# Kernel optimization log

Hardware: AMD Instinct MI355X
Metric: run time of the kernel (lower is better)

Reference implementation:

```python
import jax, jax.numpy as jnp
import numpy as np

RES = 16; NC = 256; NCP = 1024; KNN = 32; SIGMA = 0.1
DM = 256; NH = 8; FF = 1024; NLAYERS = 2
E = NC * 8 * (RES // 8) ** 2
EH = 8
B = 4; N = 65536


def setup_inputs() -> dict:
    key = jax.random.key(0)
    ks = jax.random.split(key, 16)
    s = 0.02
    def w(k, shape):
        return jax.random.normal(k, shape, jnp.float32) * s
    inp = {}
    inp['pc'] = jax.random.normal(ks[0], (B, N, 3), jnp.float32)
    inp['pe_w1'] = w(ks[1], (3, 128)); inp['pe_b1'] = jnp.zeros((128,), jnp.float32)
    inp['pe_w2'] = w(ks[2], (128, 128)); inp['pe_b2'] = jnp.zeros((128,), jnp.float32)
    inp['t_qkv_w'] = w(ks[3], (NLAYERS, DM, 3 * DM)); inp['t_qkv_b'] = jnp.zeros((NLAYERS, 3 * DM), jnp.float32)
    inp['t_out_w'] = w(ks[4], (NLAYERS, DM, DM)); inp['t_out_b'] = jnp.zeros((NLAYERS, DM), jnp.float32)
    inp['t_ln1_s'] = jnp.ones((NLAYERS, DM), jnp.float32); inp['t_ln1_b'] = jnp.zeros((NLAYERS, DM), jnp.float32)
    inp['t_ff1_w'] = w(ks[5], (NLAYERS, DM, FF)); inp['t_ff1_b'] = jnp.zeros((NLAYERS, FF), jnp.float32)
    inp['t_ff2_w'] = w(ks[6], (NLAYERS, FF, DM)); inp['t_ff2_b'] = jnp.zeros((NLAYERS, DM), jnp.float32)
    inp['t_ln2_s'] = jnp.ones((NLAYERS, DM), jnp.float32); inp['t_ln2_b'] = jnp.zeros((NLAYERS, DM), jnp.float32)
    inp['c1_w'] = w(ks[7], (2 * NC, NC, 3, 3)); inp['c1_b'] = jnp.zeros((2 * NC,), jnp.float32)
    inp['c2_w'] = w(ks[8], (4 * NC, 2 * NC, 3, 3)); inp['c2_b'] = jnp.zeros((4 * NC,), jnp.float32)
    inp['c3_w'] = w(ks[9], (8 * NC, 4 * NC, 3, 3)); inp['c3_b'] = jnp.zeros((8 * NC,), jnp.float32)
    inp['x_qkv_w'] = w(ks[10], (E, 3 * E)); inp['x_qkv_b'] = jnp.zeros((3 * E,), jnp.float32)
    inp['x_out_w'] = w(ks[11], (E, E)); inp['x_out_b'] = jnp.zeros((E,), jnp.float32)
    return inp


def _layernorm(x, s, b):
    m = x.mean(-1, keepdims=True)
    v = ((x - m) ** 2).mean(-1, keepdims=True)
    return (x - m) / jnp.sqrt(v + 1e-5) * s + b


def _mha(x, qkv_w, qkv_b, out_w, out_b, nh):
    Bq, S, D = x.shape
    dh = D // nh
    qkv = x @ qkv_w + qkv_b
    q, k, v = jnp.split(qkv, 3, axis=-1)
    def sp(t):
        return t.reshape(Bq, S, nh, dh).transpose(0, 2, 1, 3)
    q, k, v = sp(q), sp(k), sp(v)
    a = jax.nn.softmax(jnp.einsum('bhqd,bhkd->bhqk', q, k) / jnp.sqrt(jnp.float32(dh)), axis=-1)
    o = jnp.einsum('bhqk,bhkd->bhqd', a, v).transpose(0, 2, 1, 3).reshape(Bq, S, D)
    return o @ out_w + out_b


def _density(pc):
    # faithful to source: distance to the FIRST k points (unsorted), not kNN
    d = jnp.linalg.norm(pc[:, :, None, :] - pc[:, None, :KNN, :], axis=-1)  # (B,N,k)
    return jnp.exp(-2.0 * SIGMA ** 2 / (d * d + 1e-6)).mean(axis=-1)


def _fps_indices(pc, density):
    # incremental min-dist FPS: selects identical points to the original O(N*K^2) loop
    def one(pc_b, dens_b):
        first = jnp.argmax(dens_b)
        mind = jnp.linalg.norm(pc_b - pc_b[first], axis=-1)
        def step(mind, _):
            idx = jnp.argmax(mind)
            d = jnp.linalg.norm(pc_b - pc_b[idx], axis=-1)
            return jnp.minimum(mind, d), idx
        _, rest = jax.lax.scan(step, mind, None, length=NCP - 1)
        return jnp.concatenate([first[None], rest])
    return jax.vmap(one)(pc, density)


def _forward(pc, idx, pe_w1, pe_b1, pe_w2, pe_b2, t_qkv_w, t_qkv_b, t_out_w, t_out_b,
             t_ln1_s, t_ln1_b, t_ff1_w, t_ff1_b, t_ff2_w, t_ff2_b, t_ln2_s, t_ln2_b,
             c1_w, c1_b, c2_w, c2_b, c3_w, c3_b, x_qkv_w, x_qkv_b, x_out_w, x_out_b):
    Bq = pc.shape[0]
    centers = jnp.take_along_axis(pc, idx[:, :, None], axis=1)  # (B,K,3)
    # point encoder MLP -> (B,K,128)
    f = jax.nn.relu(centers @ pe_w1 + pe_b1) @ pe_w2 + pe_b2
    # sinusoidal pos-emb per axis, mean over xyz -> (B,K,128)
    half = 64
    freqs = jnp.exp(jnp.arange(half, dtype=jnp.float32) * (-np.log(10000.0) / (half - 1)))
    e = centers[..., None] * freqs  # (B,K,3,64)
    pos = jnp.concatenate([jnp.sin(e), jnp.cos(e)], axis=-1).mean(axis=2)
    x = jnp.concatenate([f, pos], axis=-1)  # (B,K,256)
    # 2-layer post-LN transformer encoder
    for l in range(NLAYERS):
        h = _mha(x, t_qkv_w[l], t_qkv_b[l], t_out_w[l], t_out_b[l], NH)
        x = _layernorm(x + h, t_ln1_s[l], t_ln1_b[l])
        h = jax.nn.relu(x @ t_ff1_w[l] + t_ff1_b[l]) @ t_ff2_w[l] + t_ff2_b[l]
        x = _layernorm(x + h, t_ln2_s[l], t_ln2_b[l])
    # scatter-add features onto three planes
    L = pc.max() - pc.min()
    def grid(c):
        return jnp.clip(((c + L / 2) / L * RES).astype(jnp.int32), 0, RES - 1)
    gx = grid(centers[..., 0]); gy = grid(centers[..., 1]); gz = grid(centers[..., 2])
    tri = jnp.zeros((Bq, 3, RES, RES, DM), jnp.float32)  # channels last for scatter
    bi = jnp.arange(Bq)[:, None]
    tri = tri.at[bi, 0, gy, gx].add(x)
    tri = tri.at[bi, 1, gz, gy].add(x)
    tri = tri.at[bi, 2, gz, gx].add(x)
    tri = tri.transpose(0, 1, 4, 2, 3)  # (B,3,C,R,R)
    z = tri.reshape(Bq * 3, DM, RES, RES)
    def conv(xx, w, b):
        y = jax.lax.conv_general_dilated(xx, w, (2, 2), ((1, 1), (1, 1)),
                                         dimension_numbers=('NCHW', 'OIHW', 'NCHW'))
        return y + b[None, :, None, None]
    z = jax.nn.relu(conv(z, c1_w, c1_b))
    z = jax.nn.relu(conv(z, c2_w, c2_b))
    z = jax.nn.relu(conv(z, c3_w, c3_b))  # (B*3, 8C, R/8, R/8)
    flat = z.reshape(Bq, 3, E)
    attn = _mha(flat, x_qkv_w, x_qkv_b, x_out_w, x_out_b, EH)
    return attn.reshape(Bq, 3, 8 * NC, RES // 8, RES // 8)


def reference(pc, pe_w1, pe_b1, pe_w2, pe_b2, t_qkv_w, t_qkv_b, t_out_w, t_out_b,
              t_ln1_s, t_ln1_b, t_ff1_w, t_ff1_b, t_ff2_w, t_ff2_b, t_ln2_s, t_ln2_b,
              c1_w, c1_b, c2_w, c2_b, c3_w, c3_b, x_qkv_w, x_qkv_b, x_out_w, x_out_b):
    idx = _fps_indices(pc, _density(pc))
    return _forward(pc, idx, pe_w1, pe_b1, pe_w2, pe_b2, t_qkv_w, t_qkv_b, t_out_w, t_out_b,
                    t_ln1_s, t_ln1_b, t_ff1_w, t_ff1_b, t_ff2_w, t_ff2_b, t_ln2_s, t_ln2_b,
                    c1_w, c1_b, c2_w, c2_b, c3_w, c3_b, x_qkv_w, x_qkv_b, x_out_w, x_out_b)
```

## Files before the change

kernel.cpp:

```cpp
#include <hip/hip_runtime.h>
#include <math.h>

#define NPTS   65536
#define NBATCH 4
#define KCP    1024
#define DM     256
#define FFD    1024
#define EDIM   8192
#define N3E    24576

#define FPS_NBLK 16
#define FPS_THR  256
#define FPS_PPT  16
#define GPUB     8
#define HARV_MAX 16
#define RING     16
#define TSPLIT   512

typedef __attribute__((ext_vector_type(8))) short short8v;
typedef __attribute__((ext_vector_type(4))) short short4v;
typedef __attribute__((ext_vector_type(4))) float float4v;

__device__ __forceinline__ unsigned long long umaxll(unsigned long long a, unsigned long long b) {
  return a > b ? a : b;
}

__device__ __forceinline__ short bf16rn(float f) {
  unsigned u = __float_as_uint(f);
  return (short)((u + 0x7FFFu + ((u >> 16) & 1u)) >> 16);
}

__global__ __launch_bounds__(256) void redmm_kernel(const float* __restrict__ v, int n,
                                                    float* __restrict__ pmax, float* __restrict__ pmin) {
  float mx = -INFINITY, mn = INFINITY;
  for (int i = blockIdx.x * 256 + threadIdx.x; i < n; i += gridDim.x * 256) {
    float x = v[i]; mx = fmaxf(mx, x); mn = fminf(mn, x);
  }
#pragma unroll
  for (int off = 32; off >= 1; off >>= 1) {
    mx = fmaxf(mx, __shfl_xor(mx, off, 64));
    mn = fminf(mn, __shfl_xor(mn, off, 64));
  }
  __shared__ float smx[4], smn[4];
  int lane = threadIdx.x & 63, w = threadIdx.x >> 6;
  if (lane == 0) { smx[w] = mx; smn[w] = mn; }
  __syncthreads();
  if (threadIdx.x == 0) {
    pmax[blockIdx.x] = fmaxf(fmaxf(smx[0], smx[1]), fmaxf(smx[2], smx[3]));
    pmin[blockIdx.x] = fminf(fminf(smn[0], smn[1]), fminf(smn[2], smn[3]));
  }
}

__global__ __launch_bounds__(256) void redfin_kernel(const float* __restrict__ pmax,
                                                     const float* __restrict__ pmin, int nb,
                                                     float* __restrict__ Lv) {
  float mx = -INFINITY, mn = INFINITY;
  for (int i = threadIdx.x; i < nb; i += 256) { mx = fmaxf(mx, pmax[i]); mn = fminf(mn, pmin[i]); }
#pragma unroll
  for (int off = 32; off >= 1; off >>= 1) {
    mx = fmaxf(mx, __shfl_xor(mx, off, 64));
    mn = fminf(mn, __shfl_xor(mn, off, 64));
  }
  __shared__ float smx[4], smn[4];
  int lane = threadIdx.x & 63, w = threadIdx.x >> 6;
  if (lane == 0) { smx[w] = mx; smn[w] = mn; }
  __syncthreads();
  if (threadIdx.x == 0) {
    mx = fmaxf(fmaxf(smx[0], smx[1]), fmaxf(smx[2], smx[3]));
    mn = fminf(fminf(smn[0], smn[1]), fminf(smn[2], smn[3]));
    Lv[0] = __fsub_rn(mx, mn);
  }
}

__global__ __launch_bounds__(FPS_THR, 1) void fps_kernel(const float* __restrict__ pc,
                                                         float* __restrict__ centers,
                                                         unsigned* __restrict__ tags,
                                                         unsigned long long* __restrict__ keys,
                                                         float* __restrict__ mindbuf,
                                                         int* __restrict__ state,
                                                         int phase) {
  const int blk = blockIdx.x;
  const int b = blk / FPS_NBLK, bb = blk % FPS_NBLK;
  const int tid = threadIdx.x;
  const int lane = tid & 63, wv = tid >> 6;
  const int wvg = bb * 4 + wv;
  const float* pcb = pc + (size_t)b * NPTS * 3;

  __shared__ float kpts[96];
  __shared__ float wlds[2][HARV_MAX][3];
  __shared__ int hcnt[2];

  float px[FPS_PPT], py[FPS_PPT], pz[FPS_PPT], mind[FPS_PPT];
  const int gbase = wvg * 1024;
#pragma unroll
  for (int i = 0; i < FPS_PPT; ++i) {
    int g = gbase + i * 64 + lane;
    px[i] = pcb[3 * g]; py[i] = pcb[3 * g + 1]; pz[i] = pcb[3 * g + 2];
  }

  unsigned* const tagb = tags + (size_t)b * RING * 64;
  unsigned long long* const keyb = keys + (size_t)b * RING * 64 * GPUB;
  float* const mb = mindbuf + ((size_t)b * 64 + wvg) * FPS_PPT * 64;

  int t, r;
  if (phase == 0) {
    for (int i = tid; i < 96; i += FPS_THR) kpts[i] = pcb[i];
    __syncthreads();
    unsigned long long bk = 0ull;
#pragma unroll
    for (int i = 0; i < FPS_PPT; ++i) {
      float acc = 0.f;
      for (int j = 0; j < 32; ++j) {
        float dx = __fsub_rn(px[i], kpts[3 * j]);
        float dy = __fsub_rn(py[i], kpts[3 * j + 1]);
        float dz = __fsub_rn(pz[i], kpts[3 * j + 2]);
        float ss = __fadd_rn(__fadd_rn(__fmul_rn(dx, dx), __fmul_rn(dy, dy)), __fmul_rn(dz, dz));
        float d = __fsqrt_rn(ss);
        float dd = __fadd_rn(__fmul_rn(d, d), 1e-6f);
        acc = __fadd_rn(acc, expf(__fdiv_rn(-0.02f, dd)));
      }
      float dens = __fdiv_rn(acc, 32.f);
      int g = gbase + i * 64 + lane;
      bk = umaxll(bk, ((unsigned long long)__float_as_uint(dens) << 32) | (unsigned int)(~g));
    }
#pragma unroll
    for (int off = 1; off < 64; off <<= 1) bk = umaxll(bk, __shfl_xor(bk, off, 64));
    if (lane == 0) {
      keyb[(size_t)(1 & (RING - 1)) * 64 * GPUB + wvg * GPUB] = bk;
      __hip_atomic_store(&tagb[(1 & (RING - 1)) * 64 + wvg], 1u, __ATOMIC_RELEASE, __HIP_MEMORY_SCOPE_AGENT);
    }
    unsigned tag;
    do {
      tag = __hip_atomic_load(&tagb[(1 & (RING - 1)) * 64 + lane], __ATOMIC_ACQUIRE, __HIP_MEMORY_SCOPE_AGENT);
    } while (__any(tag != 1u));
    unsigned long long k2 = __hip_atomic_load(&keyb[(size_t)(1 & (RING - 1)) * 64 * GPUB + lane * GPUB],
                                              __ATOMIC_RELAXED, __HIP_MEMORY_SCOPE_AGENT);
#pragma unroll
    for (int off = 1; off < 64; off <<= 1) k2 = umaxll(k2, __shfl_xor(k2, off, 64));
    int widx = (int)(~(unsigned)(k2 & 0xFFFFFFFFull));
    float wx = pcb[3 * widx], wy = pcb[3 * widx + 1], wz = pcb[3 * widx + 2];
    if (wvg == 0 && lane == 0) {
      centers[(size_t)b * KCP * 3 + 0] = wx;
      centers[(size_t)b * KCP * 3 + 1] = wy;
      centers[(size_t)b * KCP * 3 + 2] = wz;
    }
#pragma unroll
    for (int i = 0; i < FPS_PPT; ++i) {
      float dx = __fsub_rn(px[i], wx), dy = __fsub_rn(py[i], wy), dz = __fsub_rn(pz[i], wz);
      mind[i] = __fsqrt_rn(__fadd_rn(__fadd_rn(__fmul_rn(dx, dx), __fmul_rn(dy, dy)), __fmul_rn(dz, dz)));
    }
    t = 1; r = 2;
  } else {
    r = state[b * 2]; t = state[b * 2 + 1];
#pragma unroll
    for (int i = 0; i < FPS_PPT; ++i) mind[i] = mb[i * 64 + lane];
  }

  const int tend = phase ? KCP : TSPLIT;
  while (t < tend) {
    unsigned long long tk[FPS_PPT];
#pragma unroll
    for (int i = 0; i < FPS_PPT; ++i) {
      int g = gbase + i * 64 + lane;
      tk[i] = ((unsigned long long)__float_as_uint(mind[i]) << 32) | (unsigned int)(~g);
    }
    unsigned long long ek[GPUB];
#pragma unroll
    for (int g = 0; g < GPUB; ++g) {
      unsigned long long lbk = 0ull;
#pragma unroll
      for (int i = 0; i < FPS_PPT; ++i) lbk = umaxll(lbk, tk[i]);
      unsigned long long wk = lbk;
#pragma unroll
      for (int off = 1; off < 64; off <<= 1) wk = umaxll(wk, __shfl_xor(wk, off, 64));
      ek[g] = wk;
#pragma unroll
      for (int i = 0; i < FPS_PPT; ++i)
        if (tk[i] == wk) tk[i] = 0ull;
    }
    const int ri = r & (RING - 1);
    if (lane == 0) {
      unsigned long long* sp = keyb + ((size_t)ri * 64 + wvg) * GPUB;
#pragma unroll
      for (int g = 0; g < GPUB; ++g)
        __hip_atomic_store(&sp[g], ek[g], __ATOMIC_RELAXED, __HIP_MEMORY_SCOPE_AGENT);
      __hip_atomic_store(&tagb[ri * 64 + wvg], (unsigned)r, __ATOMIC_RELEASE, __HIP_MEMORY_SCOPE_AGENT);
    }

    if (wv == 0) {
      unsigned tag;
      do {
        tag = __hip_atomic_load(&tagb[ri * 64 + lane], __ATOMIC_ACQUIRE, __HIP_MEMORY_SCOPE_AGENT);
      } while (__any(tag != (unsigned)r));
      const unsigned long long* pl = keyb + ((size_t)ri * 64 + lane) * GPUB;
      unsigned long long ck[GPUB];
#pragma unroll
      for (int e = 0; e < GPUB; ++e)
        ck[e] = __hip_atomic_load(&pl[e], __ATOMIC_RELAXED, __HIP_MEMORY_SCOPE_AGENT);
      float cx[GPUB], cy[GPUB], cz[GPUB];
#pragma unroll
      for (int e = 0; e < GPUB; ++e) {
        int gi = (int)(~(unsigned)(ck[e] & 0xFFFFFFFFull));
        cx[e] = pcb[3 * gi]; cy[e] = pcb[3 * gi + 1]; cz[e] = pcb[3 * gi + 2];
      }
      unsigned long long u = ck[GPUB - 1];
#pragma unroll
      for (int off = 1; off < 64; off <<= 1) u = umaxll(u, __shfl_xor(u, off, 64));
      int h = 0, tl = t;
      while (true) {
        unsigned long long lb = 0ull; float lx = 0.f, ly = 0.f, lz = 0.f;
#pragma unroll
        for (int e = 0; e < GPUB; ++e)
          if (ck[e] > lb) { lb = ck[e]; lx = cx[e]; ly = cy[e]; lz = cz[e]; }
        unsigned long long wk = lb;
#pragma unroll
        for (int off = 1; off < 64; off <<= 1) wk = umaxll(wk, __shfl_xor(wk, off, 64));
        if (h > 0 && wk < u) break;
        int owner = __ffsll(__ballot(lb == wk)) - 1;
        float wx = __shfl(lx, owner, 64), wy = __shfl(ly, owner, 64), wz = __shfl(lz, owner, 64);
        if (lane == 0) {
          wlds[r & 1][h][0] = wx; wlds[r & 1][h][1] = wy; wlds[r & 1][h][2] = wz;
          if (bb == 0) {
            centers[((size_t)b * KCP + tl) * 3 + 0] = wx;
            centers[((size_t)b * KCP + tl) * 3 + 1] = wy;
            centers[((size_t)b * KCP + tl) * 3 + 2] = wz;
          }
        }
#pragma unroll
        for (int e = 0; e < GPUB; ++e) {
          float dx = __fsub_rn(cx[e], wx), dy = __fsub_rn(cy[e], wy), dz = __fsub_rn(cz[e], wz);
          float d = __fsqrt_rn(__fadd_rn(__fadd_rn(__fmul_rn(dx, dx), __fmul_rn(dy, dy)), __fmul_rn(dz, dz)));
          float ov = __uint_as_float((unsigned)(ck[e] >> 32));
          float nv = fminf(ov, d);
          ck[e] = ((unsigned long long)__float_as_uint(nv) << 32) | (ck[e] & 0xFFFFFFFFull);
        }
        ++h; ++tl;
        if (h == HARV_MAX || tl == KCP) break;
      }
      if (lane == 0) hcnt[r & 1] = h;
    }
    __syncthreads();
    const int h = hcnt[r & 1];
    for (int j = 0; j < h; ++j) {
      float wx = wlds[r & 1][j][0], wy = wlds[r & 1][j][1], wz = wlds[r & 1][j][2];
#pragma unroll
      for (int i = 0; i < FPS_PPT; ++i) {
        float dx = __fsub_rn(px[i], wx), dy = __fsub_rn(py[i], wy), dz = __fsub_rn(pz[i], wz);
        float d = __fsqrt_rn(__fadd_rn(__fadd_rn(__fmul_rn(dx, dx), __fmul_rn(dy, dy)), __fmul_rn(dz, dz)));
        mind[i] = fminf(mind[i], d);
      }
    }
    t += h; ++r;
  }

  if (phase == 0) {
#pragma unroll
    for (int i = 0; i < FPS_PPT; ++i) mb[i * 64 + lane] = mind[i];
    if (bb == 0 && wv == 0 && lane == 0) { state[b * 2] = r; state[b * 2 + 1] = t; }
  }
}

__global__ __launch_bounds__(128) void pe_kernel(const float* __restrict__ centers,
                                                 const float* __restrict__ w1, const float* __restrict__ b1,
                                                 const float* __restrict__ w2, const float* __restrict__ b2,
                                                 float* __restrict__ x) {
  const int p = blockIdx.x;
  const int d = threadIdx.x;
  __shared__ float h[128];
  __shared__ float c[3];
  if (d < 3) c[d] = centers[(size_t)p * 3 + d];
  __syncthreads();
  float hv = b1[d];
#pragma unroll
  for (int j = 0; j < 3; ++j) hv += c[j] * w1[j * 128 + d];
  hv = fmaxf(hv, 0.f);
  h[d] = hv;
  __syncthreads();
  float f = b2[d];
  for (int j = 0; j < 128; ++j) f += h[j] * w2[j * 128 + d];
  x[(size_t)p * 256 + d] = f;
  if (d < 64) {
    float fr = expf(__fmul_rn((float)d, -0.14619587892025696f));
    float ssum = 0.f, csum = 0.f;
#pragma unroll
    for (int a = 0; a < 3; ++a) {
      float e = __fmul_rn(c[a], fr);
      ssum += sinf(e); csum += cosf(e);
    }
    x[(size_t)p * 256 + 128 + d] = __fdiv_rn(ssum, 3.f);
    x[(size_t)p * 256 + 192 + d] = __fdiv_rn(csum, 3.f);
  }
}

__global__ __launch_bounds__(256) void gemm_mfma_kernel(const float* __restrict__ A,
                                                        const float* __restrict__ W,
                                                        const float* __restrict__ bias,
                                                        float* __restrict__ C,
                                                        int M, int Kd, int Nd, int relu) {
  __shared__ __align__(16) short Al[128][40];
  __shared__ __align__(16) short Wl[128][40];
  const int bm = blockIdx.y * 128, bn = blockIdx.x * 128;
  const int tid = threadIdx.x;
  const int lane = tid & 63, wv = tid >> 6;
  const int wr = wv >> 1, wc = wv & 1;
  const int l15 = lane & 15, lk = lane >> 4;

  float4v acc[4][4];
#pragma unroll
  for (int i = 0; i < 4; ++i)
#pragma unroll
    for (int j = 0; j < 4; ++j) acc[i][j] = (float4v){0.f, 0.f, 0.f, 0.f};

  for (int k0 = 0; k0 < Kd; k0 += 32) {
    __syncthreads();
#pragma unroll
    for (int i = 0; i < 4; ++i) {
      int idx = (i * 256 + tid) * 4;
      int m = idx >> 5, k = idx & 31;
      float4 v = *(const float4*)&A[(size_t)(bm + m) * Kd + k0 + k];
      short4v s = { bf16rn(v.x), bf16rn(v.y), bf16rn(v.z), bf16rn(v.w) };
      *(short4v*)&Al[m][k] = s;
    }
#pragma unroll
    for (int i = 0; i < 4; ++i) {
      int task = i * 256 + tid;
      int n = task & 127, c = task >> 7;
      short4v s;
#pragma unroll
      for (int j = 0; j < 4; ++j)
        s[j] = bf16rn(W[(size_t)(k0 + c * 4 + j) * Nd + bn + n]);
      *(short4v*)&Wl[n][c * 4] = s;
    }
    __syncthreads();
    short8v af[4], bf[4];
#pragma unroll
    for (int mf = 0; mf < 4; ++mf)
      af[mf] = *(const short8v*)&Al[wr * 64 + mf * 16 + l15][lk * 8];
#pragma unroll
    for (int nf = 0; nf < 4; ++nf)
      bf[nf] = *(const short8v*)&Wl[wc * 64 + nf * 16 + l15][lk * 8];
#pragma unroll
    for (int mf = 0; mf < 4; ++mf)
#pragma unroll
      for (int nf = 0; nf < 4; ++nf)
        acc[mf][nf] = __builtin_amdgcn_mfma_f32_16x16x32_bf16(af[mf], bf[nf], acc[mf][nf], 0, 0, 0);
  }

#pragma unroll
  for (int mf = 0; mf < 4; ++mf) {
    int row = bm + wr * 64 + mf * 16 + lk * 4;
#pragma unroll
    for (int nf = 0; nf < 4; ++nf) {
      int col = bn + wc * 64 + nf * 16 + l15;
      float bv = bias[col];
#pragma unroll
      for (int j = 0; j < 4; ++j) {
        float v = acc[mf][nf][j] + bv;
        if (relu) v = fmaxf(v, 0.f);
        C[(size_t)(row + j) * Nd + col] = v;
      }
    }
  }
}

__global__ __launch_bounds__(256, 1) void flash_mfma_kernel(const float* __restrict__ qkv,
                                                            float* __restrict__ ao) {
  const int qt = blockIdx.x, h = blockIdx.y, b = blockIdx.z;
  const int tid = threadIdx.x;
  const int lane = tid & 63, w = tid >> 6;
  const int l15 = lane & 15, lk = lane >> 4;
  const int q0 = qt * 64;

  __shared__ __align__(16) short Kc[64][40];
  __shared__ __align__(16) short Vt[32][72];
  __shared__ __align__(16) short Plds[4][16][72];

  short8v qa;
  {
    const float* qr = qkv + (size_t)(b * 1024 + q0 + w * 16 + l15) * 768 + h * 32 + lk * 8;
    float4 a = *(const float4*)qr;
    float4 c = *(const float4*)(qr + 4);
    qa = (short8v){ bf16rn(a.x), bf16rn(a.y), bf16rn(a.z), bf16rn(a.w),
                    bf16rn(c.x), bf16rn(c.y), bf16rn(c.z), bf16rn(c.w) };
  }

  float4v o0 = (float4v){0.f, 0.f, 0.f, 0.f};
  float4v o1 = (float4v){0.f, 0.f, 0.f, 0.f};
  float m_cur[4] = { -INFINITY, -INFINITY, -INFINITY, -INFINITY };
  float l_part[4] = { 0.f, 0.f, 0.f, 0.f };
  const float scale = 0.17677669529663687f;

  for (int c0 = 0; c0 < 1024; c0 += 64) {
    __syncthreads();
    {
      int key = tid >> 2, dblk = (tid & 3) * 8;
      size_t row = (size_t)(b * 1024 + c0 + key) * 768 + h * 32 + dblk;
      float4 k1 = *(const float4*)&qkv[row + 256];
      float4 k2 = *(const float4*)&qkv[row + 260];
      short8v ks = (short8v){ bf16rn(k1.x), bf16rn(k1.y), bf16rn(k1.z), bf16rn(k1.w),
                              bf16rn(k2.x), bf16rn(k2.y), bf16rn(k2.z), bf16rn(k2.w) };
      *(short8v*)&Kc[key][dblk] = ks;
      float4 v1 = *(const float4*)&qkv[row + 512];
      float4 v2 = *(const float4*)&qkv[row + 516];
      Vt[dblk + 0][key] = bf16rn(v1.x); Vt[dblk + 1][key] = bf16rn(v1.y);
      Vt[dblk + 2][key] = bf16rn(v1.z); Vt[dblk + 3][key] = bf16rn(v1.w);
      Vt[dblk + 4][key] = bf16rn(v2.x); Vt[dblk + 5][key] = bf16rn(v2.y);
      Vt[dblk + 6][key] = bf16rn(v2.z); Vt[dblk + 7][key] = bf16rn(v2.w);
    }
    __syncthreads();

    float4v s[4];
#pragma unroll
    for (int f = 0; f < 4; ++f) {
      short8v kb = *(const short8v*)&Kc[f * 16 + l15][lk * 8];
      float4v z = (float4v){0.f, 0.f, 0.f, 0.f};
      s[f] = __builtin_amdgcn_mfma_f32_16x16x32_bf16(qa, kb, z, 0, 0, 0);
    }
#pragma unroll
    for (int f = 0; f < 4; ++f)
#pragma unroll
      for (int j = 0; j < 4; ++j) s[f][j] *= scale;

    float corr[4];
#pragma unroll
    for (int j = 0; j < 4; ++j) {
      float v = fmaxf(fmaxf(s[0][j], s[1][j]), fmaxf(s[2][j], s[3][j]));
#pragma unroll
      for (int off = 1; off < 16; off <<= 1) v = fmaxf(v, __shfl_xor(v, off, 64));
      float m_new = fmaxf(m_cur[j], v);
      corr[j] = expf(m_cur[j] - m_new);
      m_cur[j] = m_new;
    }
#pragma unroll
    for (int f = 0; f < 4; ++f)
#pragma unroll
      for (int j = 0; j < 4; ++j) {
        float p = expf(s[f][j] - m_cur[j]);
        s[f][j] = p;
        Plds[w][lk * 4 + j][f * 16 + l15] = bf16rn(p);
      }
#pragma unroll
    for (int j = 0; j < 4; ++j) {
      float tsum = s[0][j] + s[1][j] + s[2][j] + s[3][j];
#pragma unroll
      for (int off = 1; off < 16; off <<= 1) tsum += __shfl_xor(tsum, off, 64);
      l_part[j] = l_part[j] * corr[j] + tsum;
      o0[j] *= corr[j];
      o1[j] *= corr[j];
    }
    asm volatile("s_waitcnt lgkmcnt(0)" ::: "memory");
    __builtin_amdgcn_sched_barrier(0);

#pragma unroll
    for (int kb = 0; kb < 2; ++kb) {
      short8v pa = *(const short8v*)&Plds[w][l15][kb * 32 + lk * 8];
      short8v vb0 = *(const short8v*)&Vt[l15][kb * 32 + lk * 8];
      short8v vb1 = *(const short8v*)&Vt[16 + l15][kb * 32 + lk * 8];
      o0 = __builtin_amdgcn_mfma_f32_16x16x32_bf16(pa, vb0, o0, 0, 0, 0);
      o1 = __builtin_amdgcn_mfma_f32_16x16x32_bf16(pa, vb1, o1, 0, 0, 0);
    }
  }

#pragma unroll
  for (int j = 0; j < 4; ++j) {
    float inv = 1.f / l_part[j];
    int q = q0 + w * 16 + lk * 4 + j;
    float* orow = ao + (size_t)(b * 1024 + q) * 256 + h * 32;
    orow[l15] = o0[j] * inv;
    orow[16 + l15] = o1[j] * inv;
  }
}

__global__ __launch_bounds__(256) void ln_kernel(const float* __restrict__ a, const float* __restrict__ r,
                                                 const float* __restrict__ sc, const float* __restrict__ bi,
                                                 float* __restrict__ out) {
  const int row = blockIdx.x * 4 + (threadIdx.x >> 6);
  const int lane = threadIdx.x & 63;
  const float* ar = a + (size_t)row * 256;
  const float* rr = r + (size_t)row * 256;
  float v[4];
#pragma unroll
  for (int i = 0; i < 4; ++i) v[i] = ar[lane + 64 * i] + rr[lane + 64 * i];
  float s = v[0] + v[1] + v[2] + v[3];
#pragma unroll
  for (int off = 32; off >= 1; off >>= 1) s += __shfl_xor(s, off, 64);
  float mean = s * (1.f / 256.f);
  float vs = 0.f;
#pragma unroll
  for (int i = 0; i < 4; ++i) { float d = v[i] - mean; vs += d * d; }
#pragma unroll
  for (int off = 32; off >= 1; off >>= 1) vs += __shfl_xor(vs, off, 64);
  float var = vs * (1.f / 256.f);
  float rstd = 1.f / sqrtf(var + 1e-5f);
  float* orow = out + (size_t)row * 256;
#pragma unroll
  for (int i = 0; i < 4; ++i) {
    int d = lane + 64 * i;
    orow[d] = (v[i] - mean) * rstd * sc[d] + bi[d];
  }
}

__global__ __launch_bounds__(256) void scatter_kernel(const float* __restrict__ x,
                                                      const float* __restrict__ centers,
                                                      const float* __restrict__ Lv,
                                                      float* __restrict__ tri) {
  const int pnt = blockIdx.x;
  const int b = pnt >> 10;
  const int tid = threadIdx.x;
  __shared__ int g[3];
  if (tid == 0) {
    float L = Lv[0];
    float half = __fmul_rn(L, 0.5f);
#pragma unroll
    for (int a = 0; a < 3; ++a) {
      float c = centers[(size_t)pnt * 3 + a];
      float t = __fmul_rn(__fdiv_rn(__fadd_rn(c, half), L), 16.f);
      int gi = (int)t;
      g[a] = min(15, max(0, gi));
    }
  }
  __syncthreads();
  const int gx = g[0], gy = g[1], gz = g[2];
  float v = x[(size_t)pnt * 256 + tid];
  float* trib = tri + (size_t)b * 3 * 256 * 256;
  atomicAdd(&trib[(0 * 256 + tid) * 256 + gy * 16 + gx], v);
  atomicAdd(&trib[(1 * 256 + tid) * 256 + gz * 16 + gy], v);
  atomicAdd(&trib[(2 * 256 + tid) * 256 + gz * 16 + gx], v);
}

template <int IC, int OC, int IH, int IW, int OH, int OW, int OCT, int ICC>
__global__ __launch_bounds__(256, 1) void conv_kernel(const float* __restrict__ in, const float* __restrict__ w,
                                                      const float* __restrict__ bias, float* __restrict__ out) {
  __shared__ float lin[ICC * IH * IW];
  const int n = blockIdx.x;
  const int oc = blockIdx.y * OCT + threadIdx.x / (OH * OW);
  const int sp = threadIdx.x % (OH * OW);
  const int oy = sp / OW, ox = sp % OW;
  const int iy0 = oy * 2 - 1, ix0 = ox * 2 - 1;
  float acc = 0.f;
  for (int c0 = 0; c0 < IC; c0 += ICC) {
    __syncthreads();
    for (int i = threadIdx.x; i < ICC * IH * IW; i += 256)
      lin[i] = in[((size_t)n * IC + c0) * (IH * IW) + i];
    __syncthreads();
    const float* wp = w + ((size_t)oc * IC + c0) * 9;
    for (int ic = 0; ic < ICC; ++ic) {
      const float* wr = wp + (size_t)ic * 9;
      const float* lr = lin + ic * IH * IW;
#pragma unroll
      for (int ky = 0; ky < 3; ++ky) {
        int iy = iy0 + ky;
        if (iy >= 0 && iy < IH) {
#pragma unroll
          for (int kx = 0; kx < 3; ++kx) {
            int ix = ix0 + kx;
            if (ix >= 0 && ix < IW) acc += lr[iy * IW + ix] * wr[ky * 3 + kx];
          }
        }
      }
    }
  }
  out[((size_t)n * OC + oc) * (OH * OW) + sp] = fmaxf(acc + bias[oc], 0.f);
}

template <int M, int KC>
__global__ __launch_bounds__(256, 1) void matvec_part_kernel(const float* __restrict__ A,
                                                             const float* __restrict__ W,
                                                             float* __restrict__ part,
                                                             int Kd, int Nd) {
  __shared__ float Al[KC * M];
  const int tid = threadIdx.x;
  const int n = blockIdx.x * 256 + tid;
  const int k0 = blockIdx.y * KC;
  for (int i = tid; i < KC * M; i += 256) {
    int k = i / M, m = i - k * M;
    Al[i] = A[(size_t)m * Kd + k0 + k];
  }
  __syncthreads();
  float acc[M] = {};
  for (int k = 0; k < KC; ++k) {
    float wv = W[(size_t)(k0 + k) * Nd + n];
#pragma unroll
    for (int m = 0; m < M; ++m) acc[m] += Al[k * M + m] * wv;
  }
  float* pp = part + ((size_t)blockIdx.y * M) * Nd;
#pragma unroll
  for (int m = 0; m < M; ++m) pp[(size_t)m * Nd + n] = acc[m];
}

__global__ __launch_bounds__(256) void redsum_kernel(const float* __restrict__ part,
                                                     const float* __restrict__ bias,
                                                     float* __restrict__ out, int Nd, int total) {
  int i = blockIdx.x * 256 + threadIdx.x;
  if (i < total) {
    int n = i % Nd;
    float s = bias[n];
#pragma unroll
    for (int c = 0; c < 16; ++c) s += part[(size_t)c * total + i];
    out[i] = s;
  }
}

__global__ __launch_bounds__(256) void attn3_kernel(const float* __restrict__ qkv, float* __restrict__ o) {
  const int b = blockIdx.x >> 3, h = blockIdx.x & 7;
  const float* base = qkv + (size_t)b * 3 * N3E;
  const int qo = h * 1024, ko = EDIM + h * 1024, vo = 2 * EDIM + h * 1024;
  float p[9] = {};
  for (int d = threadIdx.x; d < 1024; d += 256) {
    float q0 = base[qo + d], q1 = base[N3E + qo + d], q2 = base[2 * N3E + qo + d];
    float k0 = base[ko + d], k1 = base[N3E + ko + d], k2 = base[2 * N3E + ko + d];
    p[0] += q0 * k0; p[1] += q0 * k1; p[2] += q0 * k2;
    p[3] += q1 * k0; p[4] += q1 * k1; p[5] += q1 * k2;
    p[6] += q2 * k0; p[7] += q2 * k1; p[8] += q2 * k2;
  }
  __shared__ float red[4][9];
  __shared__ float aw[9];
  const int lane = threadIdx.x & 63, w = threadIdx.x >> 6;
#pragma unroll
  for (int e = 0; e < 9; ++e)
#pragma unroll
    for (int off = 32; off >= 1; off >>= 1) p[e] += __shfl_xor(p[e], off, 64);
  if (lane == 0)
#pragma unroll
    for (int e = 0; e < 9; ++e) red[w][e] = p[e];
  __syncthreads();
  if (threadIdx.x == 0) {
    float s[9];
#pragma unroll
    for (int e = 0; e < 9; ++e) s[e] = (red[0][e] + red[1][e] + red[2][e] + red[3][e]) / 32.f;
#pragma unroll
    for (int i = 0; i < 3; ++i) {
      float m = fmaxf(fmaxf(s[i * 3], s[i * 3 + 1]), s[i * 3 + 2]);
      float e0 = expf(s[i * 3] - m), e1 = expf(s[i * 3 + 1] - m), e2 = expf(s[i * 3 + 2] - m);
      float sm = e0 + e1 + e2;
      aw[i * 3] = e0 / sm; aw[i * 3 + 1] = e1 / sm; aw[i * 3 + 2] = e2 / sm;
    }
  }
  __syncthreads();
  for (int d = threadIdx.x; d < 1024; d += 256) {
    float v0 = base[vo + d], v1 = base[N3E + vo + d], v2 = base[2 * N3E + vo + d];
#pragma unroll
    for (int i = 0; i < 3; ++i)
      o[(size_t)(b * 3 + i) * EDIM + h * 1024 + d] = aw[i * 3] * v0 + aw[i * 3 + 1] * v1 + aw[i * 3 + 2] * v2;
  }
}

extern "C" void kernel_launch(void* const* d_in, const int* in_sizes, int n_in,
                              void* d_out, int out_size, void* d_ws, size_t ws_size,
                              hipStream_t stream) {
  const float* pc      = (const float*)d_in[0];
  const float* pe_w1   = (const float*)d_in[1];
  const float* pe_b1   = (const float*)d_in[2];
  const float* pe_w2   = (const float*)d_in[3];
  const float* pe_b2   = (const float*)d_in[4];
  const float* t_qkv_w = (const float*)d_in[5];
  const float* t_qkv_b = (const float*)d_in[6];
  const float* t_out_w = (const float*)d_in[7];
  const float* t_out_b = (const float*)d_in[8];
  const float* t_ln1_s = (const float*)d_in[9];
  const float* t_ln1_b = (const float*)d_in[10];
  const float* t_ff1_w = (const float*)d_in[11];
  const float* t_ff1_b = (const float*)d_in[12];
  const float* t_ff2_w = (const float*)d_in[13];
  const float* t_ff2_b = (const float*)d_in[14];
  const float* t_ln2_s = (const float*)d_in[15];
  const float* t_ln2_b = (const float*)d_in[16];
  const float* c1_w    = (const float*)d_in[17];
  const float* c1_b    = (const float*)d_in[18];
  const float* c2_w    = (const float*)d_in[19];
  const float* c2_b    = (const float*)d_in[20];
  const float* c3_w    = (const float*)d_in[21];
  const float* c3_b    = (const float*)d_in[22];
  const float* x_qkv_w = (const float*)d_in[23];
  const float* x_qkv_b = (const float*)d_in[24];
  const float* x_out_w = (const float*)d_in[25];
  const float* x_out_b = (const float*)d_in[26];
  float* outp = (float*)d_out;

  char* wsp = (char*)d_ws;
  auto alloc = [&](size_t bytes) { char* q = wsp; wsp += (bytes + 255) & ~(size_t)255; return q; };
  float* centers = (float*)alloc((size_t)NBATCH * KCP * 3 * 4);
  float* pmax    = (float*)alloc(512 * 4);
  float* pmin    = (float*)alloc(512 * 4);
  float* Lv      = (float*)alloc(256);
  unsigned* tags = (unsigned*)alloc((size_t)NBATCH * RING * 64 * 4);
  unsigned long long* keyss = (unsigned long long*)alloc((size_t)NBATCH * RING * 64 * GPUB * 8);
  float* mindbuf = (float*)alloc((size_t)NBATCH * NPTS * 4);
  int* fstate    = (int*)alloc(256);
  float* x  = (float*)alloc((size_t)4096 * 256 * 4);
  float* xb = (float*)alloc((size_t)4096 * 256 * 4);
  float* arena = (float*)wsp;
  float* qkvb = arena;
  float* ao   = qkvb + (size_t)4096 * 768;
  float* po   = ao + (size_t)4096 * 256;
  float* ffh  = po + (size_t)4096 * 256;
  float* ffo  = ffh + (size_t)4096 * 1024;
  float* tri  = arena;
  float* z1   = tri + (size_t)NBATCH * 3 * 256 * 256;
  float* z2   = z1 + (size_t)12 * 512 * 64;
  float* z3   = z2 + (size_t)12 * 1024 * 16;
  float* qkv2 = z3 + (size_t)12 * 8192;
  float* at2  = qkv2 + (size_t)12 * N3E;
  float* mvp  = at2 + (size_t)12 * EDIM;
  (void)in_sizes; (void)n_in; (void)out_size; (void)ws_size; (void)ffo;

  hipMemsetAsync(tags, 0, (size_t)NBATCH * RING * 64 * 4 + (size_t)NBATCH * RING * 64 * GPUB * 8, stream);

  redmm_kernel<<<512, 256, 0, stream>>>(pc, NBATCH * NPTS * 3, pmax, pmin);
  redfin_kernel<<<1, 256, 0, stream>>>(pmax, pmin, 512, Lv);

  fps_kernel<<<NBATCH * FPS_NBLK, FPS_THR, 0, stream>>>(pc, centers, tags, keyss, mindbuf, fstate, 0);
  fps_kernel<<<NBATCH * FPS_NBLK, FPS_THR, 0, stream>>>(pc, centers, tags, keyss, mindbuf, fstate, 1);

  pe_kernel<<<NBATCH * KCP, 128, 0, stream>>>(centers, pe_w1, pe_b1, pe_w2, pe_b2, x);

  for (int l = 0; l < 2; ++l) {
    gemm_mfma_kernel<<<dim3(6, 32), 256, 0, stream>>>(x, t_qkv_w + (size_t)l * 256 * 768,
                                                      t_qkv_b + (size_t)l * 768, qkvb, 4096, 256, 768, 0);
    flash_mfma_kernel<<<dim3(16, 8, 4), 256, 0, stream>>>(qkvb, ao);
    gemm_mfma_kernel<<<dim3(2, 32), 256, 0, stream>>>(ao, t_out_w + (size_t)l * 256 * 256,
                                                      t_out_b + (size_t)l * 256, po, 4096, 256, 256, 0);
    ln_kernel<<<1024, 256, 0, stream>>>(x, po, t_ln1_s + (size_t)l * 256, t_ln1_b + (size_t)l * 256, xb);
    gemm_mfma_kernel<<<dim3(8, 32), 256, 0, stream>>>(xb, t_ff1_w + (size_t)l * 256 * 1024,
                                                      t_ff1_b + (size_t)l * 1024, ffh, 4096, 256, 1024, 1);
    gemm_mfma_kernel<<<dim3(2, 32), 256, 0, stream>>>(ffh, t_ff2_w + (size_t)l * 1024 * 256,
                                                      t_ff2_b + (size_t)l * 256, ffo, 4096, 1024, 256, 0);
    ln_kernel<<<1024, 256, 0, stream>>>(xb, ffo, t_ln2_s + (size_t)l * 256, t_ln2_b + (size_t)l * 256, x);
  }

  hipMemsetAsync(tri, 0, (size_t)NBATCH * 3 * 256 * 256 * 4, stream);
  scatter_kernel<<<NBATCH * KCP, 256, 0, stream>>>(x, centers, Lv, tri);

  conv_kernel<256, 512, 16, 16, 8, 8, 4, 32><<<dim3(12, 128), 256, 0, stream>>>(tri, c1_w, c1_b, z1);
  conv_kernel<512, 1024, 8, 8, 4, 4, 16, 128><<<dim3(12, 64), 256, 0, stream>>>(z1, c2_w, c2_b, z2);
  conv_kernel<1024, 2048, 4, 4, 2, 2, 64, 256><<<dim3(12, 32), 256, 0, stream>>>(z2, c3_w, c3_b, z3);

  matvec_part_kernel<12, 512><<<dim3(N3E / 256, 16), 256, 0, stream>>>(z3, x_qkv_w, mvp, EDIM, N3E);
  redsum_kernel<<<(12 * N3E + 255) / 256, 256, 0, stream>>>(mvp, x_qkv_b, qkv2, N3E, 12 * N3E);

  attn3_kernel<<<32, 256, 0, stream>>>(qkv2, at2);

  matvec_part_kernel<12, 512><<<dim3(EDIM / 256, 16), 256, 0, stream>>>(at2, x_out_w, mvp, EDIM, EDIM);
  redsum_kernel<<<(12 * EDIM + 255) / 256, 256, 0, stream>>>(mvp, x_out_b, outp, EDIM, 12 * EDIM);
}
```

Before: 4.503 ms.

## Restructure conv3 to reuse weights across batch and vectorize matvec weight loads

The third conv layer gets its own kernel. Each thread owns one output channel and spatial position and accumulates all 12 images, staging input channel slices in shared memory so each weight is loaded once and reused 12 times. The matvec kernels now read weights as float4 and each thread handles four output columns, which cuts grid size by four. This targets the weight-bandwidth-bound tail, but the conv3 grid shrinks to 32 blocks and the matvec to 24 or 8 by 16 blocks, so far fewer CUs may be occupied.

```diff
diff --git a/kernel.cpp b/kernel.cpp
--- a/kernel.cpp
+++ b/kernel.cpp
@@ -563,29 +563,84 @@
   out[((size_t)n * OC + oc) * (OH * OW) + sp] = fmaxf(acc + bias[oc], 0.f);
 }
 
+__global__ __launch_bounds__(256, 1) void conv3w_kernel(const float* __restrict__ in,
+                                                        const float* __restrict__ w,
+                                                        const float* __restrict__ bias,
+                                                        float* __restrict__ out) {
+  __shared__ float lin[12][128][16];
+  const int oc = blockIdx.x * 64 + (threadIdx.x >> 2);
+  const int sp = threadIdx.x & 3;
+  const int oy = sp >> 1, ox = sp & 1;
+  const int iy0 = oy * 2 - 1, ix0 = ox * 2 - 1;
+  float acc[12] = {};
+  for (int c0 = 0; c0 < 1024; c0 += 128) {
+    __syncthreads();
+    for (int i = threadIdx.x; i < 6144; i += 256) {
+      int n = i / 512, r4 = i - n * 512;
+      ((float4*)&lin[n][0][0])[r4] = ((const float4*)(in + ((size_t)n * 1024 + c0) * 16))[r4];
+    }
+    __syncthreads();
+    const float* wp = w + ((size_t)oc * 1024 + c0) * 9;
+    for (int ic = 0; ic < 128; ++ic) {
+      const float* wr = wp + (size_t)ic * 9;
+      float wv[9];
+#pragma unroll
+      for (int q = 0; q < 9; ++q) wv[q] = wr[q];
+#pragma unroll
+      for (int n = 0; n < 12; ++n) {
+        const float* lr = &lin[n][ic][0];
+        float a = acc[n];
+#pragma unroll
+        for (int ky = 0; ky < 3; ++ky) {
+          int iy = iy0 + ky;
+          if (iy >= 0 && iy < 4) {
+#pragma unroll
+            for (int kx = 0; kx < 3; ++kx) {
+              int ix = ix0 + kx;
+              if (ix >= 0 && ix < 4) a += lr[iy * 4 + ix] * wv[ky * 3 + kx];
+            }
+          }
+        }
+        acc[n] = a;
+      }
+    }
+  }
+  float bv = bias[oc];
+#pragma unroll
+  for (int n = 0; n < 12; ++n)
+    out[((size_t)n * 2048 + oc) * 4 + sp] = fmaxf(acc[n] + bv, 0.f);
+}
+
 template <int M, int KC>
-__global__ __launch_bounds__(256, 1) void matvec_part_kernel(const float* __restrict__ A,
-                                                             const float* __restrict__ W,
-                                                             float* __restrict__ part,
-                                                             int Kd, int Nd) {
+__global__ __launch_bounds__(256, 1) void matvec_part4_kernel(const float* __restrict__ A,
+                                                              const float* __restrict__ W,
+                                                              float* __restrict__ part,
+                                                              int Kd, int Nd) {
   __shared__ float Al[KC * M];
   const int tid = threadIdx.x;
-  const int n = blockIdx.x * 256 + tid;
+  const int n4 = blockIdx.x * 256 + tid;
+  const int nd4 = Nd >> 2;
   const int k0 = blockIdx.y * KC;
   for (int i = tid; i < KC * M; i += 256) {
     int k = i / M, m = i - k * M;
     Al[i] = A[(size_t)m * Kd + k0 + k];
   }
   __syncthreads();
-  float acc[M] = {};
+  float4 acc[M];
+#pragma unroll
+  for (int m = 0; m < M; ++m) acc[m] = make_float4(0.f, 0.f, 0.f, 0.f);
+  const float4* W4 = (const float4*)W;
   for (int k = 0; k < KC; ++k) {
-    float wv = W[(size_t)(k0 + k) * Nd + n];
-#pragma unroll
-    for (int m = 0; m < M; ++m) acc[m] += Al[k * M + m] * wv;
-  }
-  float* pp = part + ((size_t)blockIdx.y * M) * Nd;
-#pragma unroll
-  for (int m = 0; m < M; ++m) pp[(size_t)m * Nd + n] = acc[m];
+    float4 wv = W4[(size_t)(k0 + k) * nd4 + n4];
+#pragma unroll
+    for (int m = 0; m < M; ++m) {
+      float a = Al[k * M + m];
+      acc[m].x += a * wv.x; acc[m].y += a * wv.y; acc[m].z += a * wv.z; acc[m].w += a * wv.w;
+    }
+  }
+  float4* pp = (float4*)(part + ((size_t)blockIdx.y * M) * Nd);
+#pragma unroll
+  for (int m = 0; m < M; ++m) pp[(size_t)m * nd4 + n4] = acc[m];
 }
 
 __global__ __launch_bounds__(256) void redsum_kernel(const float* __restrict__ part,
@@ -733,13 +788,13 @@
 
   conv_kernel<256, 512, 16, 16, 8, 8, 4, 32><<<dim3(12, 128), 256, 0, stream>>>(tri, c1_w, c1_b, z1);
   conv_kernel<512, 1024, 8, 8, 4, 4, 16, 128><<<dim3(12, 64), 256, 0, stream>>>(z1, c2_w, c2_b, z2);
-  conv_kernel<1024, 2048, 4, 4, 2, 2, 64, 256><<<dim3(12, 32), 256, 0, stream>>>(z2, c3_w, c3_b, z3);
-
-  matvec_part_kernel<12, 512><<<dim3(N3E / 256, 16), 256, 0, stream>>>(z3, x_qkv_w, mvp, EDIM, N3E);
+  conv3w_kernel<<<32, 256, 0, stream>>>(z2, c3_w, c3_b, z3);
+
+  matvec_part4_kernel<12, 512><<<dim3(N3E / 1024, 16), 256, 0, stream>>>(z3, x_qkv_w, mvp, EDIM, N3E);
   redsum_kernel<<<(12 * N3E + 255) / 256, 256, 0, stream>>>(mvp, x_qkv_b, qkv2, N3E, 12 * N3E);
 
   attn3_kernel<<<32, 256, 0, stream>>>(qkv2, at2);
 
-  matvec_part_kernel<12, 512><<<dim3(EDIM / 256, 16), 256, 0, stream>>>(at2, x_out_w, mvp, EDIM, EDIM);
+  matvec_part4_kernel<12, 512><<<dim3(EDIM / 1024, 16), 256, 0, stream>>>(at2, x_out_w, mvp, EDIM, EDIM);
   redsum_kernel<<<(12 * EDIM + 255) / 256, 256, 0, stream>>>(mvp, x_out_b, outp, EDIM, 12 * EDIM);
 }
```

Result: slower. 6.596 ms (+46.5%).
